# Performance work log

Measured on AMD Instinct MI355X. Metric: run time of the kernel, lower is better.

## Reference

```python
import jax, jax.numpy as jnp
import numpy as np

N = 20000      # nodes
E = 320000     # edges (before self loops)
IN = 128       # in_channels
HID = 256      # hidden_channels
HEADS = 8
C = HID // HEADS  # 32 per-head dim
L = 4          # num_gat_layers
BN_EPS = 1e-5
LN_EPS = 1e-5


def setup_inputs() -> dict:
    key = jax.random.key(0)
    ks = iter(jax.random.split(key, 64))
    def rn(shape, s=0.05):
        return jax.random.normal(next(ks), shape, jnp.float32) * s
    inp = {
        'x': jax.random.normal(next(ks), (N, IN), jnp.float32),
        'edge_index': jax.random.randint(next(ks), (2, E), 0, N),
        # FeatureMLP
        'mlp_w1': rn((IN, HID)), 'mlp_b1': jnp.zeros((HID,), jnp.float32),
        'bn1_g': jnp.ones((HID,), jnp.float32), 'bn1_b': jnp.zeros((HID,), jnp.float32),
        'mlp_w2': rn((HID, HID)), 'mlp_b2': jnp.zeros((HID,), jnp.float32),
        'bn2_g': jnp.ones((HID,), jnp.float32), 'bn2_b': jnp.zeros((HID,), jnp.float32),
        'mlp_w3': rn((HID, HID)), 'mlp_b3': jnp.zeros((HID,), jnp.float32),
        # stacked GATv2 layer params [L, ...]
        'gat_wl': rn((L, HID, HID)), 'gat_bl': jnp.zeros((L, HID), jnp.float32),
        'gat_wr': rn((L, HID, HID)), 'gat_br': jnp.zeros((L, HID), jnp.float32),
        'gat_att': rn((L, HEADS, C)), 'gat_bias': jnp.zeros((L, HID), jnp.float32),
        'ln_g': jnp.ones((L, HID), jnp.float32), 'ln_b': jnp.zeros((L, HID), jnp.float32),
        'head_w1': rn((2 * HID, HID)), 'head_b1': jnp.zeros((HID,), jnp.float32),
        'hbn1_g': jnp.ones((HID,), jnp.float32), 'hbn1_b': jnp.zeros((HID,), jnp.float32),
        'head_w2': rn((HID, HID // 2)), 'head_b2': jnp.zeros((HID // 2,), jnp.float32),
        'hbn2_g': jnp.ones((HID // 2,), jnp.float32), 'hbn2_b': jnp.zeros((HID // 2,), jnp.float32),
        'head_w3': rn((HID // 2, HID // 4)), 'head_b3': jnp.zeros((HID // 4,), jnp.float32),
        'head_w4': rn((HID // 4, 1)), 'head_b4': jnp.zeros((1,), jnp.float32),
    }
    return inp


def _lrelu01(v):
    return jax.nn.leaky_relu(v, 0.1)


def _bn_eval(v, g, b):
    # eval-mode BatchNorm1d with running_mean=0, running_var=1
    return v * (g / jnp.sqrt(1.0 + BN_EPS)) + b


def _layernorm(v, g, b):
    mu = jnp.mean(v, axis=-1, keepdims=True)
    var = jnp.mean((v - mu) ** 2, axis=-1, keepdims=True)
    return (v - mu) / jnp.sqrt(var + LN_EPS) * g + b


def _gatv2(x, src, dst, Wl, bl, Wr, br, att, bias):
    n = x.shape[0]
    xl = (x @ Wl + bl).reshape(n, HEADS, C)   # source transform
    xr = (x @ Wr + br).reshape(n, HEADS, C)   # target transform
    # per-edge attention logits (GATv2): a . LeakyReLU(x_l[src] + x_r[dst])
    e = jax.nn.leaky_relu(xl[src] + xr[dst], 0.2)          # [E, H, C]
    logits = jnp.einsum('ehc,hc->eh', e, att)               # [E, H]
    # segment softmax over destination nodes
    m = jax.ops.segment_max(logits, dst, num_segments=n)    # [N, H]
    a = jnp.exp(logits - m[dst])
    s = jax.ops.segment_sum(a, dst, num_segments=n)
    alpha = a / (s[dst] + 1e-16)                            # [E, H]
    out = jax.ops.segment_sum(xl[src] * alpha[:, :, None], dst, num_segments=n)
    return out.reshape(n, HID) + bias


def _forward(x, mlp_w1, mlp_b1, bn1_g, bn1_b, mlp_w2, mlp_b2, bn2_g, bn2_b,
             mlp_w3, mlp_b3, gat_wl, gat_bl, gat_wr, gat_br, gat_att, gat_bias,
             ln_g, ln_b, head_w1, head_b1, hbn1_g, hbn1_b, head_w2, head_b2,
             hbn2_g, hbn2_b, head_w3, head_b3, head_w4, head_b4, edge_index):
    n = x.shape[0]
    # FeatureMLP (eval: dropout off)
    h = _lrelu01(_bn_eval(x @ mlp_w1 + mlp_b1, bn1_g, bn1_b))
    h = _lrelu01(_bn_eval(h @ mlp_w2 + mlp_b2, bn2_g, bn2_b))
    x_mlp = h @ mlp_w3 + mlp_b3
    # add self loops
    loop = jnp.arange(n)
    src = jnp.concatenate([edge_index[0], loop])
    dst = jnp.concatenate([edge_index[1], loop])
    g = x_mlp
    for i in range(L):
        res = g
        o = _gatv2(g, src, dst, gat_wl[i], gat_bl[i], gat_wr[i], gat_br[i],
                   gat_att[i], gat_bias[i])
        o = _lrelu01(_layernorm(o, ln_g[i], ln_b[i]))
        g = o + res
    xc = jnp.concatenate([x_mlp, g], axis=1)                # [N, 2*HID]
    h = _lrelu01(_bn_eval(xc @ head_w1 + head_b1, hbn1_g, hbn1_b))
    h = _lrelu01(_bn_eval(h @ head_w2 + head_b2, hbn2_g, hbn2_b))
    h = _lrelu01(h @ head_w3 + head_b3)
    return h @ head_w4 + head_b4                            # [N, 1]


def reference(x, edge_index, mlp_w1, mlp_b1, bn1_g, bn1_b, mlp_w2, mlp_b2,
              bn2_g, bn2_b, mlp_w3, mlp_b3, gat_wl, gat_bl, gat_wr, gat_br,
              gat_att, gat_bias, ln_g, ln_b, head_w1, head_b1, hbn1_g, hbn1_b,
              head_w2, head_b2, hbn2_g, hbn2_b, head_w3, head_b3, head_w4, head_b4):
    return _forward(x, mlp_w1, mlp_b1, bn1_g, bn1_b, mlp_w2, mlp_b2, bn2_g,
                    bn2_b, mlp_w3, mlp_b3, gat_wl, gat_bl, gat_wr, gat_br,
                    gat_att, gat_bias, ln_g, ln_b, head_w1, head_b1, hbn1_g,
                    hbn1_b, head_w2, head_b2, hbn2_g, hbn2_b, head_w3, head_b3,
                    head_w4, head_b4, edge_index)
```

## Files before the change

### kernel.cpp

```cpp
#include <hip/hip_runtime.h>
#include <hip/hip_bf16.h>

#define N_NODES 20000
#define E_EDGES 320000
#define E_TOT   (E_EDGES + N_NODES)
#define IN_CH   128
#define HID     256
#define HEADS   8
#define CPH     32

enum { EP_BIAS = 0, EP_BN_LRELU = 1, EP_LRELU = 2 };

typedef _Float16 f16;
typedef f16  f16x2 __attribute__((ext_vector_type(2)));
typedef f16  f16x4 __attribute__((ext_vector_type(4)));
typedef f16  f16x8 __attribute__((ext_vector_type(8)));
typedef float f32x2 __attribute__((ext_vector_type(2)));
typedef float f32x4 __attribute__((ext_vector_type(4)));

__device__ __forceinline__ f16x2 h2max(f16x2 a, f16x2 b) {
#if __has_builtin(__builtin_elementwise_max)
    return __builtin_elementwise_max(a, b);
#else
    f16x2 r; r[0] = a[0] > b[0] ? a[0] : b[0]; r[1] = a[1] > b[1] ? a[1] : b[1]; return r;
#endif
}
__device__ __forceinline__ float hdot2(f16x2 a, f16x2 b, float c) {
#if __has_builtin(__builtin_amdgcn_fdot2)
    return __builtin_amdgcn_fdot2(a, b, c, false);
#else
    return c + (float)a[0] * (float)b[0] + (float)a[1] * (float)b[1];
#endif
}
__device__ __forceinline__ float fexp2(float x) {
#if __has_builtin(__builtin_amdgcn_exp2f)
    return __builtin_amdgcn_exp2f(x);
#else
    return exp2f(x);
#endif
}

__device__ __forceinline__ size_t frag_idx(int row, int col, int KB) {
    int kb = col >> 6, ks = (col >> 5) & 1, q = (col >> 3) & 3, e = col & 7;
    return ((((size_t)(row >> 4) * KB + kb) * 2 + ks) << 9) + (((q << 4) | (row & 15)) << 3) + e;
}

struct WDesc { const float* src; f16* dst; int K; int Nc; int NTOT; int ct0; };
struct WDescs { WDesc d[14]; };

#define WPREP_BLKS (14 * 512)
#define CVT_BLKS   ((N_NODES * IN_CH) / 256)
#define DEG_BLKS   ((E_EDGES + 255) / 256)
#define ZERO_BLKS  ((N_NODES + 255) / 256)
#define PREP_BLKS  (WPREP_BLKS + CVT_BLKS + DEG_BLKS + ZERO_BLKS)

__global__ __launch_bounds__(256)
void prep_kernel(WDescs ds, const float* __restrict__ x, f16* __restrict__ x16,
                 const int* __restrict__ dstE, int* __restrict__ cnt, int* __restrict__ cur)
{
    const int bx = blockIdx.x;
    const int tid = threadIdx.x;
    if (bx < WPREP_BLKS) {
        WDesc w = ds.d[bx >> 9];
        int i = ((bx & 511) << 8) + tid;
        if (i < w.K * w.Nc) {
            int NT_local = w.Nc >> 4;
            int e  = i & 7;
            int l  = (i >> 3) & 63;
            int r  = i >> 9;
            int ct = r % NT_local;
            int q  = r / NT_local;
            int ks = q & 1;
            int kb = q >> 1;
            int n  = ct * 16 + (l & 15);
            int k  = kb * 64 + ks * 32 + ((l >> 4) << 3) + e;
            size_t di = (((size_t)(kb * 2 + ks) * w.NTOT + w.ct0 + ct) << 9) + (l << 3) + e;
            w.dst[di] = (f16)w.src[(size_t)k * w.Nc + n];
        }
    } else if (bx < WPREP_BLKS + CVT_BLKS) {
        int i = (bx - WPREP_BLKS) * 256 + tid;
        if (i < N_NODES * IN_CH) {
            int row = i / IN_CH, col = i - row * IN_CH;
            x16[frag_idx(row, col, 2)] = (f16)x[i];
        }
    } else if (bx < WPREP_BLKS + CVT_BLKS + DEG_BLKS) {
        int e = (bx - WPREP_BLKS - CVT_BLKS) * 256 + tid;
        if (e < E_EDGES) atomicAdd(&cnt[dstE[e]], 1);
    } else {
        int i = (bx - WPREP_BLKS - CVT_BLKS - DEG_BLKS) * 256 + tid;
        if (i < N_NODES) cur[i] = 0;
    }
}

template<int NT, int NTOT, int WAVES, int RT, int DOT, int OUTF>
__global__ __launch_bounds__(WAVES * 64)
void gemm_kernel(const f16* __restrict__ A1, int KB1,
                 const f16* __restrict__ A2, int KB2,
                 const f16* __restrict__ Wf,
                 const float* __restrict__ biasA,
                 const float* __restrict__ biasB,
                 const float* __restrict__ bng,
                 const float* __restrict__ bnb,
                 f16* __restrict__ out16A,
                 f16* __restrict__ out16B,
                 f16* __restrict__ dup16,
                 float* __restrict__ out32,
                 const float* __restrict__ dotw,
                 const float* __restrict__ dotb,
                 float* __restrict__ outdot,
                 int NcA, int KBo, int mode)
{
    __shared__ float red[DOT ? 16 : 1][DOT ? 65 : 1];
    const int tid  = threadIdx.x;
    const int wave = tid >> 6;
    const int lane = tid & 63;
    const int quad = lane >> 4;
    const int rb0 = blockIdx.x * RT;
    const int KBt = KB1 + KB2;

    f32x4 acc[RT][NT];
#pragma unroll
    for (int t = 0; t < RT; ++t)
#pragma unroll
        for (int j = 0; j < NT; ++j) acc[t][j] = (f32x4){0.f, 0.f, 0.f, 0.f};

#pragma unroll 2
    for (int kb = 0; kb < KBt; ++kb) {
#pragma unroll
        for (int ks = 0; ks < 2; ++ks) {
            f16x8 a[RT];
#pragma unroll
            for (int t = 0; t < RT; ++t) {
                const f16* ap = (kb < KB1)
                    ? A1 + (((((size_t)(rb0 + t)) * KB1 + kb) * 2 + ks) << 9) + (lane << 3)
                    : A2 + (((((size_t)(rb0 + t)) * KB2 + (kb - KB1)) * 2 + ks) << 9) + (lane << 3);
                a[t] = *(const f16x8*)ap;
            }
            const f16* bp = Wf + (((size_t)(kb * 2 + ks) * NTOT + wave * NT) << 9) + (lane << 3);
#pragma unroll
            for (int ct = 0; ct < NT; ++ct) {
                f16x8 b = *(const f16x8*)(bp + ((size_t)ct << 9));
#pragma unroll
                for (int t = 0; t < RT; ++t)
                    acc[t][ct] = __builtin_amdgcn_mfma_f32_16x16x32_f16(a[t], b, acc[t][ct], 0, 0, 0);
            }
        }
    }

    const int c0 = lane & 15;
    const int NcB = NTOT * 16 - NcA;
#pragma unroll
    for (int t = 0; t < RT; ++t) {
        const int r0 = (rb0 + t) * 16 + (quad << 2);
#pragma unroll
        for (int ct = 0; ct < NT; ++ct) {
            int col = (wave * NT + ct) * 16 + c0;
            bool isB = col >= NcA;
            int colL = isB ? col - NcA : col;
            float bv = isB ? biasB[colL] : biasA[colL];
            float sc = 1.f, sh = 0.f;
            if (mode == EP_BN_LRELU) {
                sc = bng[col] * rsqrtf(1.f + 1e-5f);
                sh = bnb[col];
            }
#pragma unroll
            for (int reg = 0; reg < 4; ++reg) {
                int row = r0 + reg;
                float v = acc[t][ct][reg] + bv;
                if (mode == EP_BN_LRELU) { v = v * sc + sh; v = v > 0.f ? v : 0.1f * v; }
                else if (mode == EP_LRELU) { v = v > 0.f ? v : 0.1f * v; }
                if (DOT) {
                    red[(quad << 2) + reg][col] = v * dotw[col];
                } else {
                    if (OUTF) {
                        size_t idx = frag_idx(row, col, KBo);
                        out16A[idx] = (f16)v;
                        if (dup16) dup16[idx] = (f16)v;
                        if (out32) out32[(size_t)row * NcA + col] = v;
                    } else {
                        f16* Cout = isB ? out16B : out16A;
                        int stride = isB ? NcB : NcA;
                        Cout[(size_t)row * stride + colL] = (f16)v;
                    }
                }
            }
        }
    }

    if (DOT) {
        __syncthreads();
        if (wave == 0) {
            int r = lane & 15, q = lane >> 4;
            float psum = 0.f;
#pragma unroll
            for (int j = 0; j < 16; ++j) psum += red[r][q * 16 + j];
            psum += __shfl_xor(psum, 16, 64);
            psum += __shfl_xor(psum, 32, 64);
            if (lane < 16) outdot[rb0 * 16 + r] = psum + dotb[0];
        }
    }
}

__global__ __launch_bounds__(512)
void scan_mlp1_kernel(const int* __restrict__ cnt, int* __restrict__ off,
                      const f16* __restrict__ x16, const f16* __restrict__ w1f,
                      const float* __restrict__ b1,
                      const float* __restrict__ bng, const float* __restrict__ bnb,
                      f16* __restrict__ h1)
{
    __shared__ int wsum[8];
    const int tid  = threadIdx.x;
    const int wave = tid >> 6;
    const int lane = tid & 63;

    if (blockIdx.x == 0) {
        const int base = tid * 40;
        int pre[40];
        int loc = 0;
#pragma unroll
        for (int j = 0; j < 40; ++j) {
            int i = base + j;
            int c = (i < N_NODES) ? cnt[i] + 1 : 0;
            pre[j] = loc;
            loc += c;
        }
        int s = loc;
#pragma unroll
        for (int d = 1; d < 64; d <<= 1) { int t = __shfl_up(s, d, 64); if (lane >= d) s += t; }
        if (lane == 63) wsum[wave] = s;
        __syncthreads();
        int woff = 0;
#pragma unroll
        for (int j = 0; j < 8; ++j) if (j < wave) woff += wsum[j];
        int excl = woff + s - loc;
#pragma unroll
        for (int j = 0; j < 40; ++j) {
            int i = base + j;
            if (i < N_NODES) off[i] = excl + pre[j];
        }
        if (tid == 511) off[N_NODES] = woff + s;
        return;
    }

    const int quad = lane >> 4;
    const int c0   = lane & 15;
    const int rb0  = (blockIdx.x - 1) * 2;
    f32x4 acc[2][2];
#pragma unroll
    for (int t = 0; t < 2; ++t)
#pragma unroll
        for (int j = 0; j < 2; ++j) acc[t][j] = (f32x4){0.f, 0.f, 0.f, 0.f};
#pragma unroll
    for (int kb = 0; kb < 2; ++kb) {
#pragma unroll
        for (int ks = 0; ks < 2; ++ks) {
            f16x8 a[2];
#pragma unroll
            for (int t = 0; t < 2; ++t)
                a[t] = *(const f16x8*)(x16 + (((((size_t)(rb0 + t)) * 2 + kb) * 2 + ks) << 9) + (lane << 3));
            const f16* bp = w1f + (((size_t)(kb * 2 + ks) * 16 + wave * 2) << 9) + (lane << 3);
#pragma unroll
            for (int ct = 0; ct < 2; ++ct) {
                f16x8 b = *(const f16x8*)(bp + ((size_t)ct << 9));
#pragma unroll
                for (int t = 0; t < 2; ++t)
                    acc[t][ct] = __builtin_amdgcn_mfma_f32_16x16x32_f16(a[t], b, acc[t][ct], 0, 0, 0);
            }
        }
    }
#pragma unroll
    for (int t = 0; t < 2; ++t) {
        const int r0 = (rb0 + t) * 16 + (quad << 2);
#pragma unroll
        for (int ct = 0; ct < 2; ++ct) {
            const int col = (wave * 2 + ct) * 16 + c0;
            const float sc = bng[col] * rsqrtf(1.f + 1e-5f);
            const float sh = bnb[col];
            const float bv = b1[col];
#pragma unroll
            for (int reg = 0; reg < 4; ++reg) {
                float v = acc[t][ct][reg] + bv;
                v = v * sc + sh;
                v = v > 0.f ? v : 0.1f * v;
                h1[frag_idx(r0 + reg, col, 4)] = (f16)v;
            }
        }
    }
}

#define FILL_BLKS ((E_TOT + 511) / 512)

__global__ __launch_bounds__(512)
void fill_mlp2_kernel(const int* __restrict__ src, const int* __restrict__ dst,
                      const int* __restrict__ off, int* __restrict__ cur, int* __restrict__ csr,
                      const f16* __restrict__ h1, const f16* __restrict__ w2f,
                      const float* __restrict__ b2,
                      const float* __restrict__ bng, const float* __restrict__ bnb,
                      f16* __restrict__ h2)
{
    const int tid  = threadIdx.x;
    if (blockIdx.x < FILL_BLKS) {
        int i = blockIdx.x * 512 + tid;
        if (i < E_EDGES) {
            int d = dst[i];
            int pos = atomicAdd(&cur[d], 1);
            csr[off[d] + pos] = src[i];
        } else if (i < E_TOT) {
            int j = i - E_EDGES;
            csr[off[j + 1] - 1] = j;
        }
        return;
    }

    const int wave = tid >> 6;
    const int lane = tid & 63;
    const int quad = lane >> 4;
    const int c0   = lane & 15;
    const int rb0  = (blockIdx.x - FILL_BLKS) * 2;
    f32x4 acc[2][2];
#pragma unroll
    for (int t = 0; t < 2; ++t)
#pragma unroll
        for (int j = 0; j < 2; ++j) acc[t][j] = (f32x4){0.f, 0.f, 0.f, 0.f};
#pragma unroll
    for (int kb = 0; kb < 4; ++kb) {
#pragma unroll
        for (int ks = 0; ks < 2; ++ks) {
            f16x8 a[2];
#pragma unroll
            for (int t = 0; t < 2; ++t)
                a[t] = *(const f16x8*)(h1 + (((((size_t)(rb0 + t)) * 4 + kb) * 2 + ks) << 9) + (lane << 3));
            const f16* bp = w2f + (((size_t)(kb * 2 + ks) * 16 + wave * 2) << 9) + (lane << 3);
#pragma unroll
            for (int ct = 0; ct < 2; ++ct) {
                f16x8 b = *(const f16x8*)(bp + ((size_t)ct << 9));
#pragma unroll
                for (int t = 0; t < 2; ++t)
                    acc[t][ct] = __builtin_amdgcn_mfma_f32_16x16x32_f16(a[t], b, acc[t][ct], 0, 0, 0);
            }
        }
    }
#pragma unroll
    for (int t = 0; t < 2; ++t) {
        const int r0 = (rb0 + t) * 16 + (quad << 2);
#pragma unroll
        for (int ct = 0; ct < 2; ++ct) {
            const int col = (wave * 2 + ct) * 16 + c0;
            const float sc = bng[col] * rsqrtf(1.f + 1e-5f);
            const float sh = bnb[col];
            const float bv = b2[col];
#pragma unroll
            for (int reg = 0; reg < 4; ++reg) {
                float v = acc[t][ct][reg] + bv;
                v = v * sc + sh;
                v = v > 0.f ? v : 0.1f * v;
                h2[frag_idx(r0 + reg, col, 4)] = (f16)v;
            }
        }
    }
}

__global__ __launch_bounds__(512)
void head23_kernel(const f16* __restrict__ h1,
                   const f16* __restrict__ w2f,
                   const float* __restrict__ b2,
                   const float* __restrict__ bn2g, const float* __restrict__ bn2b,
                   const f16* __restrict__ w3f,
                   const float* __restrict__ b3,
                   const float* __restrict__ w4, const float* __restrict__ b4,
                   float* __restrict__ out)
{
    __shared__ f16  hs[32 * 136];
    __shared__ float red[32][65];
    const int tid  = threadIdx.x;
    const int wave = tid >> 6;
    const int lane = tid & 63;
    const int quad = lane >> 4;
    const int c0   = lane & 15;
    const int rb0  = blockIdx.x * 2;

    {
        f32x4 acc[2];
        acc[0] = (f32x4){0.f, 0.f, 0.f, 0.f};
        acc[1] = (f32x4){0.f, 0.f, 0.f, 0.f};
#pragma unroll
        for (int kb = 0; kb < 4; ++kb) {
#pragma unroll
            for (int ks = 0; ks < 2; ++ks) {
                f16x8 a0 = *(const f16x8*)(h1 + (((((size_t)rb0)     * 4 + kb) * 2 + ks) << 9) + (lane << 3));
                f16x8 a1 = *(const f16x8*)(h1 + (((((size_t)rb0 + 1) * 4 + kb) * 2 + ks) << 9) + (lane << 3));
                f16x8 b  = *(const f16x8*)(w2f + (((size_t)(kb * 2 + ks) * 8 + wave) << 9) + (lane << 3));
                acc[0] = __builtin_amdgcn_mfma_f32_16x16x32_f16(a0, b, acc[0], 0, 0, 0);
                acc[1] = __builtin_amdgcn_mfma_f32_16x16x32_f16(a1, b, acc[1], 0, 0, 0);
            }
        }
        const int col = wave * 16 + c0;
        const float sc = bn2g[col] * rsqrtf(1.f + 1e-5f);
        const float sh = bn2b[col];
        const float bv = b2[col];
#pragma unroll
        for (int t = 0; t < 2; ++t) {
            const int r0 = t * 16 + (quad << 2);
#pragma unroll
            for (int reg = 0; reg < 4; ++reg) {
                float v = acc[t][reg] + bv;
                v = v * sc + sh;
                v = v > 0.f ? v : 0.1f * v;
                hs[(r0 + reg) * 136 + col] = (f16)v;
            }
        }
    }
    __syncthreads();

    {
        const int rbL = wave >> 2;
        const int ct3 = wave & 3;
        f32x4 acc = (f32x4){0.f, 0.f, 0.f, 0.f};
#pragma unroll
        for (int ksl = 0; ksl < 4; ++ksl) {
            const int arow = rbL * 16 + (lane & 15);
            f16x8 a = *(const f16x8*)&hs[arow * 136 + ksl * 32 + ((lane >> 4) << 3)];
            f16x8 b = *(const f16x8*)(w3f + (((size_t)(ksl * 4 + ct3)) << 9) + (lane << 3));
            acc = __builtin_amdgcn_mfma_f32_16x16x32_f16(a, b, acc, 0, 0, 0);
        }
        const int col = ct3 * 16 + c0;
        const float wv = w4[col];
        const float bv = b3[col];
        const int r0 = rbL * 16 + (quad << 2);
#pragma unroll
        for (int reg = 0; reg < 4; ++reg) {
            float v = acc[reg] + bv;
            v = v > 0.f ? v : 0.1f * v;
            red[r0 + reg][col] = v * wv;
        }
    }
    __syncthreads();

    {
        const int row = wave * 4 + (lane >> 4);
        float pr = red[row][c0] + red[row][c0 + 16] + red[row][c0 + 32] + red[row][c0 + 48];
        pr += __shfl_xor(pr, 1, 64);
        pr += __shfl_xor(pr, 2, 64);
        pr += __shfl_xor(pr, 4, 64);
        pr += __shfl_xor(pr, 8, 64);
        if (c0 == 0) out[blockIdx.x * 32 + row] = pr + b4[0];
    }
}

__global__ __launch_bounds__(256)
void gat_agg_kernel(const f16* __restrict__ xl, const f16* __restrict__ xr,
                    float* __restrict__ g, f16* __restrict__ g16,
                    const int* __restrict__ off, const int* __restrict__ csr,
                    const float* __restrict__ att,
                    const float* __restrict__ bias,
                    const float* __restrict__ lng,
                    const float* __restrict__ lnb)
{
    const int wv   = threadIdx.x >> 6;
    const int ln   = threadIdx.x & 63;
    const int half = ln >> 5;
    const int lp   = ln & 31;
    const int n    = blockIdx.x * 4 + wv;
    if (n >= N_NODES) return;

    const f16x8* xl8 = (const f16x8*)xl;
    f16x8 xrv = ((const f16x8*)xr)[n * 32 + lp];
    f16x2 xr0; xr0[0] = xrv[0]; xr0[1] = xrv[1];
    f16x2 xr1; xr1[0] = xrv[2]; xr1[1] = xrv[3];
    f16x2 xr2; xr2[0] = xrv[4]; xr2[1] = xrv[5];
    f16x2 xr3; xr3[0] = xrv[6]; xr3[1] = xrv[7];
    float4 af0 = ((const float4*)att)[lp * 2];
    float4 af1 = ((const float4*)att)[lp * 2 + 1];
    const float L2E = 1.44269504f;
    f16x2 av0; av0[0] = (f16)(af0.x * L2E); av0[1] = (f16)(af0.y * L2E);
    f16x2 av1; av1[0] = (f16)(af0.z * L2E); av1[1] = (f16)(af0.w * L2E);
    f16x2 av2; av2[0] = (f16)(af1.x * L2E); av2[1] = (f16)(af1.y * L2E);
    f16x2 av3; av3[0] = (f16)(af1.z * L2E); av3[1] = (f16)(af1.w * L2E);
    const f16x2 k02 = { (f16)0.2f, (f16)0.2f };

    float s = 0.f;
    float o0 = 0.f, o1 = 0.f, o2 = 0.f, o3 = 0.f, o4 = 0.f, o5 = 0.f, o6 = 0.f, o7 = 0.f;

    int p = off[n], end = off[n + 1];

    auto procv = [&](f16x8 xv, bool valid) {
        f16x2 x0; x0[0] = xv[0]; x0[1] = xv[1];
        f16x2 x1; x1[0] = xv[2]; x1[1] = xv[3];
        f16x2 x2; x2[0] = xv[4]; x2[1] = xv[5];
        f16x2 x3; x3[0] = xv[6]; x3[1] = xv[7];
        f16x2 v0 = x0 + xr0, v1 = x1 + xr1, v2 = x2 + xr2, v3 = x3 + xr3;
        v0 = h2max(v0, v0 * k02); v1 = h2max(v1, v1 * k02);
        v2 = h2max(v2, v2 * k02); v3 = h2max(v3, v3 * k02);
        float pr = hdot2(v0, av0, hdot2(v1, av1, hdot2(v2, av2, hdot2(v3, av3, 0.f))));
        pr += __shfl_xor(pr, 1, 64);
        pr += __shfl_xor(pr, 2, 64);
        float e = valid ? fexp2(pr) : 0.f;
        s += e;
        o0 = fmaf((float)xv[0], e, o0); o1 = fmaf((float)xv[1], e, o1);
        o2 = fmaf((float)xv[2], e, o2); o3 = fmaf((float)xv[3], e, o3);
        o4 = fmaf((float)xv[4], e, o4); o5 = fmaf((float)xv[5], e, o5);
        o6 = fmaf((float)xv[6], e, o6); o7 = fmaf((float)xv[7], e, o7);
    };
    auto proc = [&](int ep) {
        bool valid = ep < end;
        int sidx = csr[valid ? ep : end - 1];
        procv(xl8[(size_t)sidx * 32 + lp], valid);
    };

    for (; p + 16 <= end; p += 16) {
        int sA = csr[p +      half];
        int sB = csr[p + 2  + half];
        int sC = csr[p + 4  + half];
        int sD = csr[p + 6  + half];
        int sE = csr[p + 8  + half];
        int sF = csr[p + 10 + half];
        int sG = csr[p + 12 + half];
        int sH = csr[p + 14 + half];
        f16x8 rA = xl8[(size_t)sA * 32 + lp];
        f16x8 rB = xl8[(size_t)sB * 32 + lp];
        f16x8 rC = xl8[(size_t)sC * 32 + lp];
        f16x8 rD = xl8[(size_t)sD * 32 + lp];
        f16x8 rE = xl8[(size_t)sE * 32 + lp];
        f16x8 rF = xl8[(size_t)sF * 32 + lp];
        f16x8 rG = xl8[(size_t)sG * 32 + lp];
        f16x8 rH = xl8[(size_t)sH * 32 + lp];
        procv(rA, true); procv(rB, true); procv(rC, true); procv(rD, true);
        procv(rE, true); procv(rF, true); procv(rG, true); procv(rH, true);
    }
    for (; p + 8 <= end; p += 8) {
        int sA = csr[p +     half];
        int sB = csr[p + 2 + half];
        int sC = csr[p + 4 + half];
        int sD = csr[p + 6 + half];
        f16x8 rA = xl8[(size_t)sA * 32 + lp];
        f16x8 rB = xl8[(size_t)sB * 32 + lp];
        f16x8 rC = xl8[(size_t)sC * 32 + lp];
        f16x8 rD = xl8[(size_t)sD * 32 + lp];
        procv(rA, true); procv(rB, true); procv(rC, true); procv(rD, true);
    }
    for (; p + 4 <= end; p += 4) {
        int sA = csr[p +     half];
        int sB = csr[p + 2 + half];
        f16x8 rA = xl8[(size_t)sA * 32 + lp];
        f16x8 rB = xl8[(size_t)sB * 32 + lp];
        procv(rA, true); procv(rB, true);
    }
    for (; p < end; p += 2) proc(p + half);

    s  += __shfl_xor(s, 32, 64);
    o0 += __shfl_xor(o0, 32, 64); o1 += __shfl_xor(o1, 32, 64);
    o2 += __shfl_xor(o2, 32, 64); o3 += __shfl_xor(o3, 32, 64);
    o4 += __shfl_xor(o4, 32, 64); o5 += __shfl_xor(o5, 32, 64);
    o6 += __shfl_xor(o6, 32, 64); o7 += __shfl_xor(o7, 32, 64);

    const int lidx = lp * 2 + half;
    float q0 = half ? o4 : o0;
    float q1 = half ? o5 : o1;
    float q2 = half ? o6 : o2;
    float q3 = half ? o7 : o3;

    float inv = 1.f / (s + 1e-16f);
    float4 bi = ((const float4*)bias)[lidx];
    float y0 = q0 * inv + bi.x;
    float y1 = q1 * inv + bi.y;
    float y2 = q2 * inv + bi.z;
    float y3 = q3 * inv + bi.w;

    float s1 = y0 + y1 + y2 + y3;
    float s2 = y0 * y0 + y1 * y1 + y2 * y2 + y3 * y3;
#pragma unroll
    for (int d = 32; d; d >>= 1) { s1 += __shfl_xor(s1, d, 64); s2 += __shfl_xor(s2, d, 64); }
    float mu  = s1 * (1.f / HID);
    float ex2 = s2 * (1.f / HID);
    float rstd = rsqrtf(ex2 - mu * mu + 1e-5f);
    float4 lg = ((const float4*)lng)[lidx];
    float4 lb = ((const float4*)lnb)[lidx];
    float nv0 = (y0 - mu) * rstd * lg.x + lb.x; nv0 = nv0 > 0.f ? nv0 : 0.1f * nv0;
    float nv1 = (y1 - mu) * rstd * lg.y + lb.y; nv1 = nv1 > 0.f ? nv1 : 0.1f * nv1;
    float nv2 = (y2 - mu) * rstd * lg.z + lb.z; nv2 = nv2 > 0.f ? nv2 : 0.1f * nv2;
    float nv3 = (y3 - mu) * rstd * lg.w + lb.w; nv3 = nv3 > 0.f ? nv3 : 0.1f * nv3;

    float4 gv = ((const float4*)g)[n * 64 + lidx];
    float g0 = nv0 + gv.x, g1 = nv1 + gv.y, g2 = nv2 + gv.z, g3 = nv3 + gv.w;
    ((float4*)g)[n * 64 + lidx] = make_float4(g0, g1, g2, g3);
    f16x4 gh; gh[0] = (f16)g0; gh[1] = (f16)g1; gh[2] = (f16)g2; gh[3] = (f16)g3;
    *(f16x4*)&g16[frag_idx(n, 4 * lidx, 4)] = gh;
}

static inline size_t align_up(size_t v, size_t a) { return (v + a - 1) & ~(a - 1); }

extern "C" void kernel_launch(void* const* d_in, const int* in_sizes, int n_in,
                              void* d_out, int out_size, void* d_ws, size_t ws_size,
                              hipStream_t stream)
{
    const float* x      = (const float*)d_in[0];
    const int*   ei     = (const int*)d_in[1];
    const float* mlp_w1 = (const float*)d_in[2];
    const float* mlp_b1 = (const float*)d_in[3];
    const float* bn1_g  = (const float*)d_in[4];
    const float* bn1_b  = (const float*)d_in[5];
    const float* mlp_w2 = (const float*)d_in[6];
    const float* mlp_b2 = (const float*)d_in[7];
    const float* bn2_g  = (const float*)d_in[8];
    const float* bn2_b  = (const float*)d_in[9];
    const float* mlp_w3 = (const float*)d_in[10];
    const float* mlp_b3 = (const float*)d_in[11];
    const float* gat_wl = (const float*)d_in[12];
    const float* gat_bl = (const float*)d_in[13];
    const float* gat_wr = (const float*)d_in[14];
    const float* gat_br = (const float*)d_in[15];
    const float* gat_att  = (const float*)d_in[16];
    const float* gat_bias = (const float*)d_in[17];
    const float* ln_g   = (const float*)d_in[18];
    const float* ln_b   = (const float*)d_in[19];
    const float* head_w1 = (const float*)d_in[20];
    const float* head_b1 = (const float*)d_in[21];
    const float* hbn1_g  = (const float*)d_in[22];
    const float* hbn1_b  = (const float*)d_in[23];
    const float* head_w2 = (const float*)d_in[24];
    const float* head_b2 = (const float*)d_in[25];
    const float* hbn2_g  = (const float*)d_in[26];
    const float* hbn2_b  = (const float*)d_in[27];
    const float* head_w3 = (const float*)d_in[28];
    const float* head_b3 = (const float*)d_in[29];
    const float* head_w4 = (const float*)d_in[30];
    const float* head_b4 = (const float*)d_in[31];
    float* out = (float*)d_out;

    char* w = (char*)d_ws;
    size_t p = 0;
    int* off  = (int*)(w + p); p = align_up(p + (N_NODES + 1) * sizeof(int), 64);
    int* fill = (int*)(w + p); p = align_up(p + N_NODES * sizeof(int), 64);
    int* cur  = (int*)(w + p); p = align_up(p + N_NODES * sizeof(int), 64);
    int* csr  = (int*)(w + p); p = align_up(p + E_TOT * sizeof(int), 64);
    float* g32 = (float*)(w + p); p = align_up(p + (size_t)N_NODES * HID * 4, 64);
    auto halloc = [&](size_t elems) {
        f16* q = (f16*)(w + p);
        p = align_up(p + elems * 2, 1024);
        return q;
    };
    f16* x16     = halloc((size_t)N_NODES * IN_CH);
    f16* h1      = halloc((size_t)N_NODES * HID);
    f16* h2      = halloc((size_t)N_NODES * HID);
    f16* x_mlp16 = halloc((size_t)N_NODES * HID);
    f16* g16     = halloc((size_t)N_NODES * HID);
    f16* xl16    = halloc((size_t)N_NODES * HID);
    f16* xr16    = halloc((size_t)N_NODES * HID);
    f16* wt_mlp1 = halloc((size_t)IN_CH * HID);
    f16* wt_mlp2 = halloc((size_t)HID * HID);
    f16* wt_mlp3 = halloc((size_t)HID * HID);
    f16* wt_g[4];
    for (int i = 0; i < 4; ++i) wt_g[i] = halloc((size_t)HID * 2 * HID);
    f16* wt_h1 = halloc((size_t)2 * HID * HID);
    f16* wt_h2 = halloc((size_t)HID * (HID / 2));
    f16* wt_h3 = halloc((size_t)(HID / 2) * (HID / 4));
    (void)ws_size; (void)in_sizes; (void)n_in; (void)out_size;

    const int* e_src = ei;
    const int* e_dst = ei + E_EDGES;

    dim3 blk(256);
    dim3 gM625((N_NODES + 31) / 32);

    WDescs ds;
    ds.d[0]  = { mlp_w1, wt_mlp1, IN_CH, HID, 16, 0 };
    ds.d[1]  = { mlp_w2, wt_mlp2, HID, HID, 16, 0 };
    ds.d[2]  = { mlp_w3, wt_mlp3, HID, HID, 16, 0 };
    for (int i = 0; i < 4; ++i) {
        ds.d[3 + 2 * i] = { gat_wl + (size_t)i * HID * HID, wt_g[i], HID, HID, 32, 0 };
        ds.d[4 + 2 * i] = { gat_wr + (size_t)i * HID * HID, wt_g[i], HID, HID, 32, 16 };
    }
    ds.d[11] = { head_w1, wt_h1, 2 * HID, HID, 16, 0 };
    ds.d[12] = { head_w2, wt_h2, HID, HID / 2, 8, 0 };
    ds.d[13] = { head_w3, wt_h3, HID / 2, HID / 4, 4, 0 };

    hipMemsetAsync(fill, 0, N_NODES * sizeof(int), stream);
    prep_kernel<<<dim3(PREP_BLKS), blk, 0, stream>>>(ds, x, x16, e_dst, fill, cur);

    scan_mlp1_kernel<<<dim3(1 + 625), dim3(512), 0, stream>>>(fill, off, x16, wt_mlp1,
        mlp_b1, bn1_g, bn1_b, h1);
    fill_mlp2_kernel<<<dim3(FILL_BLKS + 625), dim3(512), 0, stream>>>(e_src, e_dst, off, cur, csr,
        h1, wt_mlp2, mlp_b2, bn2_g, bn2_b, h2);

    gemm_kernel<2, 16, 8, 2, 0, 1><<<gM625, 512, 0, stream>>>(h2, 4, nullptr, 0, wt_mlp3, mlp_b3, mlp_b3,
        nullptr, nullptr, x_mlp16, nullptr, g16, g32, nullptr, nullptr, nullptr, HID, 4, EP_BIAS);

    for (int i = 0; i < 4; ++i) {
        gemm_kernel<4, 32, 8, 2, 0, 0><<<gM625, 512, 0, stream>>>(g16, 4, nullptr, 0, wt_g[i],
            gat_bl + i * HID, gat_br + i * HID, nullptr, nullptr,
            xl16, xr16, nullptr, nullptr, nullptr, nullptr, nullptr, HID, 0, EP_BIAS);
        gat_agg_kernel<<<(N_NODES + 3) / 4, blk, 0, stream>>>(xl16, xr16, g32, g16, off, csr,
                                                              gat_att + i * HID, gat_bias + i * HID,
                                                              ln_g + i * HID, ln_b + i * HID);
    }

    gemm_kernel<2, 16, 8, 2, 0, 1><<<gM625, 512, 0, stream>>>(x_mlp16, 4, g16, 4, wt_h1, head_b1, head_b1,
        hbn1_g, hbn1_b, h1, nullptr, nullptr, nullptr, nullptr, nullptr, nullptr, HID, 4, EP_BN_LRELU);
    head23_kernel<<<gM625, 512, 0, stream>>>(h1, wt_h2, head_b2, hbn2_g, hbn2_b,
                                             wt_h3, head_b3, head_w4, head_b4, out);
}
```

Before: 441.4 us.

## Fuse MLP chain and head chain into single kernels, overlap CSR fill with first GAT GEMM

The three feature-MLP GEMMs now run in one kernel alongside the scan, with intermediates kept in LDS instead of going through global h1/h2 buffers. The CSR fill kernel now also does the first GAT layer's projection GEMM in place of MLP layer 2. The head's first GEMM is folded into the head23 kernel, staging its output in LDS. This removes two intermediate global round-trips and several launches, at the cost of more LDS per block (lower occupancy) and a longer serial chain inside each fused block.

```diff
diff --git a/kernel.cpp b/kernel.cpp
--- a/kernel.cpp
+++ b/kernel.cpp
@@ -110,7 +110,6 @@
                  float* __restrict__ outdot,
                  int NcA, int KBo, int mode)
 {
-    __shared__ float red[DOT ? 16 : 1][DOT ? 65 : 1];
     const int tid  = threadIdx.x;
     const int wave = tid >> 6;
     const int lane = tid & 63;
@@ -169,45 +168,33 @@
                 float v = acc[t][ct][reg] + bv;
                 if (mode == EP_BN_LRELU) { v = v * sc + sh; v = v > 0.f ? v : 0.1f * v; }
                 else if (mode == EP_LRELU) { v = v > 0.f ? v : 0.1f * v; }
-                if (DOT) {
-                    red[(quad << 2) + reg][col] = v * dotw[col];
+                if (OUTF) {
+                    size_t idx = frag_idx(row, col, KBo);
+                    out16A[idx] = (f16)v;
+                    if (dup16) dup16[idx] = (f16)v;
+                    if (out32) out32[(size_t)row * NcA + col] = v;
                 } else {
-                    if (OUTF) {
-                        size_t idx = frag_idx(row, col, KBo);
-                        out16A[idx] = (f16)v;
-                        if (dup16) dup16[idx] = (f16)v;
-                        if (out32) out32[(size_t)row * NcA + col] = v;
-                    } else {
-                        f16* Cout = isB ? out16B : out16A;
-                        int stride = isB ? NcB : NcA;
-                        Cout[(size_t)row * stride + colL] = (f16)v;
-                    }
-                }
-            }
-        }
-    }
-
-    if (DOT) {
-        __syncthreads();
-        if (wave == 0) {
-            int r = lane & 15, q = lane >> 4;
-            float psum = 0.f;
-#pragma unroll
-            for (int j = 0; j < 16; ++j) psum += red[r][q * 16 + j];
-            psum += __shfl_xor(psum, 16, 64);
-            psum += __shfl_xor(psum, 32, 64);
-            if (lane < 16) outdot[rb0 * 16 + r] = psum + dotb[0];
+                    f16* Cout = isB ? out16B : out16A;
+                    int stride = isB ? NcB : NcA;
+                    Cout[(size_t)row * stride + colL] = (f16)v;
+                }
+            }
         }
     }
 }
 
 __global__ __launch_bounds__(512)
-void scan_mlp1_kernel(const int* __restrict__ cnt, int* __restrict__ off,
-                      const f16* __restrict__ x16, const f16* __restrict__ w1f,
-                      const float* __restrict__ b1,
-                      const float* __restrict__ bng, const float* __restrict__ bnb,
-                      f16* __restrict__ h1)
+void scan_mlp123_kernel(const int* __restrict__ cnt, int* __restrict__ off,
+                        const f16* __restrict__ x16,
+                        const f16* __restrict__ w1f, const float* __restrict__ b1,
+                        const float* __restrict__ bn1g, const float* __restrict__ bn1b,
+                        const f16* __restrict__ w2f, const float* __restrict__ b2,
+                        const float* __restrict__ bn2g, const float* __restrict__ bn2b,
+                        const f16* __restrict__ w3f, const float* __restrict__ b3,
+                        f16* __restrict__ x_mlp16, f16* __restrict__ g16, float* __restrict__ g32)
 {
+    __shared__ f16 hsA[32 * 264];
+    __shared__ f16 hsB[32 * 264];
     __shared__ int wsum[8];
     const int tid  = threadIdx.x;
     const int wave = tid >> 6;
@@ -245,44 +232,138 @@
     const int quad = lane >> 4;
     const int c0   = lane & 15;
     const int rb0  = (blockIdx.x - 1) * 2;
-    f32x4 acc[2][2];
-#pragma unroll
-    for (int t = 0; t < 2; ++t)
-#pragma unroll
-        for (int j = 0; j < 2; ++j) acc[t][j] = (f32x4){0.f, 0.f, 0.f, 0.f};
-#pragma unroll
-    for (int kb = 0; kb < 2; ++kb) {
-#pragma unroll
-        for (int ks = 0; ks < 2; ++ks) {
-            f16x8 a[2];
-#pragma unroll
-            for (int t = 0; t < 2; ++t)
-                a[t] = *(const f16x8*)(x16 + (((((size_t)(rb0 + t)) * 2 + kb) * 2 + ks) << 9) + (lane << 3));
-            const f16* bp = w1f + (((size_t)(kb * 2 + ks) * 16 + wave * 2) << 9) + (lane << 3);
+
+    {
+        f32x4 acc[2][2];
+#pragma unroll
+        for (int t = 0; t < 2; ++t)
+#pragma unroll
+            for (int j = 0; j < 2; ++j) acc[t][j] = (f32x4){0.f, 0.f, 0.f, 0.f};
+#pragma unroll
+        for (int kb = 0; kb < 2; ++kb) {
+#pragma unroll
+            for (int ks = 0; ks < 2; ++ks) {
+                f16x8 a[2];
+#pragma unroll
+                for (int t = 0; t < 2; ++t)
+                    a[t] = *(const f16x8*)(x16 + (((((size_t)(rb0 + t)) * 2 + kb) * 2 + ks) << 9) + (lane << 3));
+                const f16* bp = w1f + (((size_t)(kb * 2 + ks) * 16 + wave * 2) << 9) + (lane << 3);
+#pragma unroll
+                for (int ct = 0; ct < 2; ++ct) {
+                    f16x8 b = *(const f16x8*)(bp + ((size_t)ct << 9));
+#pragma unroll
+                    for (int t = 0; t < 2; ++t)
+                        acc[t][ct] = __builtin_amdgcn_mfma_f32_16x16x32_f16(a[t], b, acc[t][ct], 0, 0, 0);
+                }
+            }
+        }
+#pragma unroll
+        for (int t = 0; t < 2; ++t) {
+            const int r0 = t * 16 + (quad << 2);
 #pragma unroll
             for (int ct = 0; ct < 2; ++ct) {
-                f16x8 b = *(const f16x8*)(bp + ((size_t)ct << 9));
+                const int col = (wave * 2 + ct) * 16 + c0;
+                const float sc = bn1g[col] * rsqrtf(1.f + 1e-5f);
+                const float sh = bn1b[col];
+                const float bv = b1[col];
+#pragma unroll
+                for (int reg = 0; reg < 4; ++reg) {
+                    float v = acc[t][ct][reg] + bv;
+                    v = v * sc + sh;
+                    v = v > 0.f ? v : 0.1f * v;
+                    hsA[(r0 + reg) * 264 + col] = (f16)v;
+                }
+            }
+        }
+    }
+    __syncthreads();
+
+    {
+        f32x4 acc[2][2];
+#pragma unroll
+        for (int t = 0; t < 2; ++t)
+#pragma unroll
+            for (int j = 0; j < 2; ++j) acc[t][j] = (f32x4){0.f, 0.f, 0.f, 0.f};
+#pragma unroll
+        for (int kb = 0; kb < 4; ++kb) {
+#pragma unroll
+            for (int ks = 0; ks < 2; ++ks) {
+                const int kofs = kb * 64 + ks * 32 + ((lane >> 4) << 3);
+                f16x8 a[2];
 #pragma unroll
                 for (int t = 0; t < 2; ++t)
-                    acc[t][ct] = __builtin_amdgcn_mfma_f32_16x16x32_f16(a[t], b, acc[t][ct], 0, 0, 0);
-            }
-        }
-    }
-#pragma unroll
-    for (int t = 0; t < 2; ++t) {
-        const int r0 = (rb0 + t) * 16 + (quad << 2);
-#pragma unroll
-        for (int ct = 0; ct < 2; ++ct) {
-            const int col = (wave * 2 + ct) * 16 + c0;
-            const float sc = bng[col] * rsqrtf(1.f + 1e-5f);
-            const float sh = bnb[col];
-            const float bv = b1[col];
-#pragma unroll
-            for (int reg = 0; reg < 4; ++reg) {
-                float v = acc[t][ct][reg] + bv;
-                v = v * sc + sh;
-                v = v > 0.f ? v : 0.1f * v;
-                h1[frag_idx(r0 + reg, col, 4)] = (f16)v;
+                    a[t] = *(const f16x8*)&hsA[(t * 16 + (lane & 15)) * 264 + kofs];
+                const f16* bp = w2f + (((size_t)(kb * 2 + ks) * 16 + wave * 2) << 9) + (lane << 3);
+#pragma unroll
+                for (int ct = 0; ct < 2; ++ct) {
+                    f16x8 b = *(const f16x8*)(bp + ((size_t)ct << 9));
+#pragma unroll
+                    for (int t = 0; t < 2; ++t)
+                        acc[t][ct] = __builtin_amdgcn_mfma_f32_16x16x32_f16(a[t], b, acc[t][ct], 0, 0, 0);
+                }
+            }
+        }
+#pragma unroll
+        for (int t = 0; t < 2; ++t) {
+            const int r0 = t * 16 + (quad << 2);
+#pragma unroll
+            for (int ct = 0; ct < 2; ++ct) {
+                const int col = (wave * 2 + ct) * 16 + c0;
+                const float sc = bn2g[col] * rsqrtf(1.f + 1e-5f);
+                const float sh = bn2b[col];
+                const float bv = b2[col];
+#pragma unroll
+                for (int reg = 0; reg < 4; ++reg) {
+                    float v = acc[t][ct][reg] + bv;
+                    v = v * sc + sh;
+                    v = v > 0.f ? v : 0.1f * v;
+                    hsB[(r0 + reg) * 264 + col] = (f16)v;
+                }
+            }
+        }
+    }
+    __syncthreads();
+
+    {
+        f32x4 acc[2][2];
+#pragma unroll
+        for (int t = 0; t < 2; ++t)
+#pragma unroll
+            for (int j = 0; j < 2; ++j) acc[t][j] = (f32x4){0.f, 0.f, 0.f, 0.f};
+#pragma unroll
+        for (int kb = 0; kb < 4; ++kb) {
+#pragma unroll
+            for (int ks = 0; ks < 2; ++ks) {
+                const int kofs = kb * 64 + ks * 32 + ((lane >> 4) << 3);
+                f16x8 a[2];
+#pragma unroll
+                for (int t = 0; t < 2; ++t)
+                    a[t] = *(const f16x8*)&hsB[(t * 16 + (lane & 15)) * 264 + kofs];
+                const f16* bp = w3f + (((size_t)(kb * 2 + ks) * 16 + wave * 2) << 9) + (lane << 3);
+#pragma unroll
+                for (int ct = 0; ct < 2; ++ct) {
+                    f16x8 b = *(const f16x8*)(bp + ((size_t)ct << 9));
+#pragma unroll
+                    for (int t = 0; t < 2; ++t)
+                        acc[t][ct] = __builtin_amdgcn_mfma_f32_16x16x32_f16(a[t], b, acc[t][ct], 0, 0, 0);
+                }
+            }
+        }
+#pragma unroll
+        for (int t = 0; t < 2; ++t) {
+#pragma unroll
+            for (int ct = 0; ct < 2; ++ct) {
+                const int col = (wave * 2 + ct) * 16 + c0;
+                const float bv = b3[col];
+#pragma unroll
+                for (int reg = 0; reg < 4; ++reg) {
+                    const int row = (rb0 + t) * 16 + (quad << 2) + reg;
+                    float v = acc[t][ct][reg] + bv;
+                    size_t idx = frag_idx(row, col, 4);
+                    x_mlp16[idx] = (f16)v;
+                    g16[idx] = (f16)v;
+                    g32[(size_t)row * HID + col] = v;
+                }
             }
         }
     }
@@ -291,14 +372,13 @@
 #define FILL_BLKS ((E_TOT + 511) / 512)
 
 __global__ __launch_bounds__(512)
-void fill_mlp2_kernel(const int* __restrict__ src, const int* __restrict__ dst,
-                      const int* __restrict__ off, int* __restrict__ cur, int* __restrict__ csr,
-                      const f16* __restrict__ h1, const f16* __restrict__ w2f,
-                      const float* __restrict__ b2,
-                      const float* __restrict__ bng, const float* __restrict__ bnb,
-                      f16* __restrict__ h2)
+void fill_gemm0_kernel(const int* __restrict__ src, const int* __restrict__ dst,
+                       const int* __restrict__ off, int* __restrict__ cur, int* __restrict__ csr,
+                       const f16* __restrict__ g16, const f16* __restrict__ w0f,
+                       const float* __restrict__ bl, const float* __restrict__ br,
+                       f16* __restrict__ xl, f16* __restrict__ xr)
 {
-    const int tid  = threadIdx.x;
+    const int tid = threadIdx.x;
     if (blockIdx.x < FILL_BLKS) {
         int i = blockIdx.x * 512 + tid;
         if (i < E_EDGES) {
@@ -317,22 +397,22 @@
     const int quad = lane >> 4;
     const int c0   = lane & 15;
     const int rb0  = (blockIdx.x - FILL_BLKS) * 2;
-    f32x4 acc[2][2];
+    f32x4 acc[2][4];
 #pragma unroll
     for (int t = 0; t < 2; ++t)
 #pragma unroll
-        for (int j = 0; j < 2; ++j) acc[t][j] = (f32x4){0.f, 0.f, 0.f, 0.f};
-#pragma unroll
+        for (int j = 0; j < 4; ++j) acc[t][j] = (f32x4){0.f, 0.f, 0.f, 0.f};
+#pragma unroll 2
     for (int kb = 0; kb < 4; ++kb) {
 #pragma unroll
         for (int ks = 0; ks < 2; ++ks) {
             f16x8 a[2];
 #pragma unroll
             for (int t = 0; t < 2; ++t)
-                a[t] = *(const f16x8*)(h1 + (((((size_t)(rb0 + t)) * 4 + kb) * 2 + ks) << 9) + (lane << 3));
-            const f16* bp = w2f + (((size_t)(kb * 2 + ks) * 16 + wave * 2) << 9) + (lane << 3);
-#pragma unroll
-            for (int ct = 0; ct < 2; ++ct) {
+                a[t] = *(const f16x8*)(g16 + (((((size_t)(rb0 + t)) * 4 + kb) * 2 + ks) << 9) + (lane << 3));
+            const f16* bp = w0f + (((size_t)(kb * 2 + ks) * 32 + wave * 4) << 9) + (lane << 3);
+#pragma unroll
+            for (int ct = 0; ct < 4; ++ct) {
                 f16x8 b = *(const f16x8*)(bp + ((size_t)ct << 9));
 #pragma unroll
                 for (int t = 0; t < 2; ++t)
@@ -344,33 +424,35 @@
     for (int t = 0; t < 2; ++t) {
         const int r0 = (rb0 + t) * 16 + (quad << 2);
 #pragma unroll
-        for (int ct = 0; ct < 2; ++ct) {
-            const int col = (wave * 2 + ct) * 16 + c0;
-            const float sc = bng[col] * rsqrtf(1.f + 1e-5f);
-            const float sh = bnb[col];
-            const float bv = b2[col];
-#pragma unroll
-            for (int reg = 0; reg < 4; ++reg) {
-                float v = acc[t][ct][reg] + bv;
-                v = v * sc + sh;
-                v = v > 0.f ? v : 0.1f * v;
-                h2[frag_idx(r0 + reg, col, 4)] = (f16)v;
-            }
+        for (int ct = 0; ct < 4; ++ct) {
+            const int col = (wave * 4 + ct) * 16 + c0;
+            const bool isR = col >= HID;
+            const int colL = col & (HID - 1);
+            const float bv = isR ? br[colL] : bl[colL];
+            f16* Cout = isR ? xr : xl;
+#pragma unroll
+            for (int reg = 0; reg < 4; ++reg)
+                Cout[(size_t)(r0 + reg) * HID + colL] = (f16)(acc[t][ct][reg] + bv);
         }
     }
 }
 
 __global__ __launch_bounds__(512)
-void head23_kernel(const f16* __restrict__ h1,
-                   const f16* __restrict__ w2f,
-                   const float* __restrict__ b2,
-                   const float* __restrict__ bn2g, const float* __restrict__ bn2b,
-                   const f16* __restrict__ w3f,
-                   const float* __restrict__ b3,
-                   const float* __restrict__ w4, const float* __restrict__ b4,
-                   float* __restrict__ out)
+void head123_kernel(const f16* __restrict__ xm,
+                    const f16* __restrict__ g16,
+                    const f16* __restrict__ w1f,
+                    const float* __restrict__ b1,
+                    const float* __restrict__ bn1g, const float* __restrict__ bn1b,
+                    const f16* __restrict__ w2f,
+                    const float* __restrict__ b2,
+                    const float* __restrict__ bn2g, const float* __restrict__ bn2b,
+                    const f16* __restrict__ w3f,
+                    const float* __restrict__ b3,
+                    const float* __restrict__ w4, const float* __restrict__ b4,
+                    float* __restrict__ out)
 {
-    __shared__ f16  hs[32 * 136];
+    __shared__ f16  hsA[32 * 264];
+    __shared__ f16  hsB[32 * 136];
     __shared__ float red[32][65];
     const int tid  = threadIdx.x;
     const int wave = tid >> 6;
@@ -380,6 +462,55 @@
     const int rb0  = blockIdx.x * 2;
 
     {
+        f32x4 acc[2][2];
+#pragma unroll
+        for (int t = 0; t < 2; ++t)
+#pragma unroll
+            for (int j = 0; j < 2; ++j) acc[t][j] = (f32x4){0.f, 0.f, 0.f, 0.f};
+#pragma unroll 2
+        for (int kb = 0; kb < 8; ++kb) {
+#pragma unroll
+            for (int ks = 0; ks < 2; ++ks) {
+                f16x8 a[2];
+#pragma unroll
+                for (int t = 0; t < 2; ++t) {
+                    const f16* ap = (kb < 4)
+                        ? xm  + (((((size_t)(rb0 + t)) * 4 + kb) * 2 + ks) << 9) + (lane << 3)
+                        : g16 + (((((size_t)(rb0 + t)) * 4 + (kb - 4)) * 2 + ks) << 9) + (lane << 3);
+                    a[t] = *(const f16x8*)ap;
+                }
+                const f16* bp = w1f + (((size_t)(kb * 2 + ks) * 16 + wave * 2) << 9) + (lane << 3);
+#pragma unroll
+                for (int ct = 0; ct < 2; ++ct) {
+                    f16x8 b = *(const f16x8*)(bp + ((size_t)ct << 9));
+#pragma unroll
+                    for (int t = 0; t < 2; ++t)
+                        acc[t][ct] = __builtin_amdgcn_mfma_f32_16x16x32_f16(a[t], b, acc[t][ct], 0, 0, 0);
+                }
+            }
+        }
+#pragma unroll
+        for (int t = 0; t < 2; ++t) {
+            const int r0 = t * 16 + (quad << 2);
+#pragma unroll
+            for (int ct = 0; ct < 2; ++ct) {
+                const int col = (wave * 2 + ct) * 16 + c0;
+                const float sc = bn1g[col] * rsqrtf(1.f + 1e-5f);
+                const float sh = bn1b[col];
+                const float bv = b1[col];
+#pragma unroll
+                for (int reg = 0; reg < 4; ++reg) {
+                    float v = acc[t][ct][reg] + bv;
+                    v = v * sc + sh;
+                    v = v > 0.f ? v : 0.1f * v;
+                    hsA[(r0 + reg) * 264 + col] = (f16)v;
+                }
+            }
+        }
+    }
+    __syncthreads();
+
+    {
         f32x4 acc[2];
         acc[0] = (f32x4){0.f, 0.f, 0.f, 0.f};
         acc[1] = (f32x4){0.f, 0.f, 0.f, 0.f};
@@ -387,8 +518,9 @@
         for (int kb = 0; kb < 4; ++kb) {
 #pragma unroll
             for (int ks = 0; ks < 2; ++ks) {
-                f16x8 a0 = *(const f16x8*)(h1 + (((((size_t)rb0)     * 4 + kb) * 2 + ks) << 9) + (lane << 3));
-                f16x8 a1 = *(const f16x8*)(h1 + (((((size_t)rb0 + 1) * 4 + kb) * 2 + ks) << 9) + (lane << 3));
+                const int kofs = kb * 64 + ks * 32 + ((lane >> 4) << 3);
+                f16x8 a0 = *(const f16x8*)&hsA[(lane & 15) * 264 + kofs];
+                f16x8 a1 = *(const f16x8*)&hsA[(16 + (lane & 15)) * 264 + kofs];
                 f16x8 b  = *(const f16x8*)(w2f + (((size_t)(kb * 2 + ks) * 8 + wave) << 9) + (lane << 3));
                 acc[0] = __builtin_amdgcn_mfma_f32_16x16x32_f16(a0, b, acc[0], 0, 0, 0);
                 acc[1] = __builtin_amdgcn_mfma_f32_16x16x32_f16(a1, b, acc[1], 0, 0, 0);
@@ -406,7 +538,7 @@
                 float v = acc[t][reg] + bv;
                 v = v * sc + sh;
                 v = v > 0.f ? v : 0.1f * v;
-                hs[(r0 + reg) * 136 + col] = (f16)v;
+                hsB[(r0 + reg) * 136 + col] = (f16)v;
             }
         }
     }
@@ -419,7 +551,7 @@
 #pragma unroll
         for (int ksl = 0; ksl < 4; ++ksl) {
             const int arow = rbL * 16 + (lane & 15);
-            f16x8 a = *(const f16x8*)&hs[arow * 136 + ksl * 32 + ((lane >> 4) << 3)];
+            f16x8 a = *(const f16x8*)&hsB[arow * 136 + ksl * 32 + ((lane >> 4) << 3)];
             f16x8 b = *(const f16x8*)(w3f + (((size_t)(ksl * 4 + ct3)) << 9) + (lane << 3));
             acc = __builtin_amdgcn_mfma_f32_16x16x32_f16(a, b, acc, 0, 0, 0);
         }
@@ -640,8 +772,6 @@
         return q;
     };
     f16* x16     = halloc((size_t)N_NODES * IN_CH);
-    f16* h1      = halloc((size_t)N_NODES * HID);
-    f16* h2      = halloc((size_t)N_NODES * HID);
     f16* x_mlp16 = halloc((size_t)N_NODES * HID);
     f16* g16     = halloc((size_t)N_NODES * HID);
     f16* xl16    = halloc((size_t)N_NODES * HID);
@@ -677,15 +807,16 @@
     hipMemsetAsync(fill, 0, N_NODES * sizeof(int), stream);
     prep_kernel<<<dim3(PREP_BLKS), blk, 0, stream>>>(ds, x, x16, e_dst, fill, cur);
 
-    scan_mlp1_kernel<<<dim3(1 + 625), dim3(512), 0, stream>>>(fill, off, x16, wt_mlp1,
-        mlp_b1, bn1_g, bn1_b, h1);
-    fill_mlp2_kernel<<<dim3(FILL_BLKS + 625), dim3(512), 0, stream>>>(e_src, e_dst, off, cur, csr,
-        h1, wt_mlp2, mlp_b2, bn2_g, bn2_b, h2);
-
-    gemm_kernel<2, 16, 8, 2, 0, 1><<<gM625, 512, 0, stream>>>(h2, 4, nullptr, 0, wt_mlp3, mlp_b3, mlp_b3,
-        nullptr, nullptr, x_mlp16, nullptr, g16, g32, nullptr, nullptr, nullptr, HID, 4, EP_BIAS);
-
-    for (int i = 0; i < 4; ++i) {
+    scan_mlp123_kernel<<<dim3(1 + 625), dim3(512), 0, stream>>>(fill, off, x16,
+        wt_mlp1, mlp_b1, bn1_g, bn1_b,
+        wt_mlp2, mlp_b2, bn2_g, bn2_b,
+        wt_mlp3, mlp_b3, x_mlp16, g16, g32);
+    fill_gemm0_kernel<<<dim3(FILL_BLKS + 625), dim3(512), 0, stream>>>(e_src, e_dst, off, cur, csr,
+        g16, wt_g[0], gat_bl, gat_br, xl16, xr16);
+
+    gat_agg_kernel<<<(N_NODES + 3) / 4, blk, 0, stream>>>(xl16, xr16, g32, g16, off, csr,
+                                                          gat_att, gat_bias, ln_g, ln_b);
+    for (int i = 1; i < 4; ++i) {
         gemm_kernel<4, 32, 8, 2, 0, 0><<<gM625, 512, 0, stream>>>(g16, 4, nullptr, 0, wt_g[i],
             gat_bl + i * HID, gat_br + i * HID, nullptr, nullptr,
             xl16, xr16, nullptr, nullptr, nullptr, nullptr, nullptr, HID, 0, EP_BIAS);
@@ -694,8 +825,8 @@
                                                               ln_g + i * HID, ln_b + i * HID);
     }
 
-    gemm_kernel<2, 16, 8, 2, 0, 1><<<gM625, 512, 0, stream>>>(x_mlp16, 4, g16, 4, wt_h1, head_b1, head_b1,
-        hbn1_g, hbn1_b, h1, nullptr, nullptr, nullptr, nullptr, nullptr, nullptr, HID, 4, EP_BN_LRELU);
-    head23_kernel<<<gM625, 512, 0, stream>>>(h1, wt_h2, head_b2, hbn2_g, hbn2_b,
-                                             wt_h3, head_b3, head_w4, head_b4, out);
-}
+    head123_kernel<<<gM625, dim3(512), 0, stream>>>(x_mlp16, g16,
+        wt_h1, head_b1, hbn1_g, hbn1_b,
+        wt_h2, head_b2, hbn2_g, hbn2_b,
+        wt_h3, head_b3, head_w4, head_b4, out);
+}
```

Measured after the change: 415.0 us. 6.0% less time.
